# Performance work log

Hardware: AMD Instinct MI355X
Metric: run time of the kernel (lower is better)

The kernel has to match this reference:

```python
import jax, jax.numpy as jnp
import numpy as np
from itertools import combinations as _comb
from jax import lax

RANKS_HIGH = 15
SUITS_HIGH = 5
NA = 6
M = 512
UNSPOOL_INDEX = np.array([h + b for h in _comb(range(0, 4), 2) for b in _comb(range(4, 9), 3)])  # (60,5)


def _unspool(x):
    # x: (B, M, 18) int -> sorted (B, M, 60, 5) rank/suit sequences
    ranks = x[:, :, 0::2]
    suits = x[:, :, 1::2]
    hr, hs = ranks[:, :, :4], suits[:, :, :4]
    br, bs = ranks[:, :, 4:], suits[:, :, 4:]
    hi = jnp.argsort(hs, axis=-1)
    bi = jnp.argsort(bs, axis=-1)
    hr = jnp.take_along_axis(hr, hi, axis=-1)
    hs = jnp.take_along_axis(hs, hi, axis=-1)
    br = jnp.take_along_axis(br, bi, axis=-1)
    bs = jnp.take_along_axis(bs, bi, axis=-1)
    hi2 = jnp.argsort(hr, axis=-1)
    bi2 = jnp.argsort(br, axis=-1)
    ranks_s = jnp.concatenate([jnp.take_along_axis(hr, hi2, -1), jnp.take_along_axis(br, bi2, -1)], axis=-1)
    suits_s = jnp.concatenate([jnp.take_along_axis(hs, hi2, -1), jnp.take_along_axis(bs, bi2, -1)], axis=-1)
    return ranks_s[:, :, UNSPOOL_INDEX], suits_s[:, :, UNSPOOL_INDEX]


def _bn_relu(x, g, b, eps=1e-5):
    # x: (B, M, 60, C, L); torch applies BN per (i,j) slice with batch=60,
    # so stats are over axes (60, L) independently for each (b, m).
    mu = jnp.mean(x, axis=(2, 4), keepdims=True)
    var = jnp.var(x, axis=(2, 4), keepdims=True)
    y = (x - mu) * lax.rsqrt(var + eps) * g[None, None, None, :, None] + b[None, None, None, :, None]
    return jax.nn.relu(y)


def setup_inputs() -> dict:
    key = jax.random.key(0)
    ks = jax.random.split(key, 24)
    s = 0.05
    inp = {
        "x": jax.random.randint(ks[0], (M, 18), 0, 5, dtype=jnp.int64 if jax.config.jax_enable_x64 else jnp.int32),
        "w_suit": jax.random.normal(ks[1], (16, 5), jnp.float32) * s,
        "b_suit": jnp.zeros((16,), jnp.float32),
        "g_suit": jnp.ones((16,), jnp.float32),
        "be_suit": jnp.zeros((16,), jnp.float32),
        "w_rank": jax.random.normal(ks[2], (16, 5, 5), jnp.float32) * s,
        "b_rank": jnp.zeros((16,), jnp.float32),
        "g_rank": jnp.ones((16,), jnp.float32),
        "be_rank": jnp.zeros((16,), jnp.float32),
        "w_h1": jax.random.normal(ks[3], (16, 32), jnp.float32) * s,
        "b_h1": jnp.zeros((32,), jnp.float32),
        "w_h2": jax.random.normal(ks[4], (32, 32), jnp.float32) * s,
        "b_h2": jnp.zeros((32,), jnp.float32),
        "w_cat": jax.random.normal(ks[5], (512, 7463), jnp.float32) * s,
        "b_cat": jnp.zeros((7463,), jnp.float32),
        "w_o1": jax.random.normal(ks[6], (15360, 512), jnp.float32) * 0.01,
        "b_o1": jnp.zeros((512,), jnp.float32),
        "w_o2": jax.random.normal(ks[7], (512, 256), jnp.float32) * s,
        "b_o2": jnp.zeros((256,), jnp.float32),
        "w_o3": jax.random.normal(ks[8], (256, 127), jnp.float32) * s,
        "b_o3": jnp.zeros((127,), jnp.float32),
        "w_sc": jax.random.normal(ks[9], (128, NA), jnp.float32) * s,
        "b_sc": jnp.zeros((NA,), jnp.float32),
    }
    return inp


def reference(x, w_suit, b_suit, g_suit, be_suit, w_rank, b_rank, g_rank, be_rank,
              w_h1, b_h1, w_h2, b_h2, w_cat, b_cat,
              w_o1, b_o1, w_o2, b_o2, w_o3, b_o3, w_sc, b_sc):
    x = x[None]  # (1, M, 18)
    B, Mdim, _ = x.shape
    ranks, suits = _unspool(x)  # (B,M,60,5) each
    hot_ranks = jax.nn.one_hot(ranks, RANKS_HIGH, dtype=jnp.float32)  # (B,M,60,5,15)
    hot_suits = jax.nn.one_hot(suits, SUITS_HIGH, dtype=jnp.float32)  # (B,M,60,5,5)

    # suit conv: Conv1d(5,16,k=1) == channel mixing pointwise
    s_out = jnp.einsum('bmncl,oc->bmnol', hot_suits, w_suit) + b_suit[None, None, None, :, None]
    s_out = _bn_relu(s_out, g_suit, be_suit)  # (B,M,60,16,5)

    # rank conv: Conv1d(5,16,k=5), valid padding: 15 -> 11
    xr = hot_ranks.reshape(B * Mdim * 60, 5, RANKS_HIGH)
    r = lax.conv_general_dilated(xr, w_rank, window_strides=(1,), padding='VALID',
                                 dimension_numbers=('NCH', 'OIH', 'NCH'))
    r = r.reshape(B, Mdim, 60, 16, 11) + b_rank[None, None, None, :, None]
    r_out = _bn_relu(r, g_rank, be_rank)  # (B,M,60,16,11)

    out = jnp.concatenate([r_out, s_out], axis=-1)  # (B,M,60,16,16)
    raw_flat = out.reshape(B, Mdim, 60, 256)

    h = jax.nn.relu(jnp.einsum('...i,io->...o', out, w_h1) + b_h1)
    h = jax.nn.relu(jnp.einsum('...i,io->...o', h, w_h2) + b_h2)  # (B,M,60,16,32)
    logits = jnp.einsum('bmnd,dk->bmnk', h.reshape(B, Mdim, 60, 512), w_cat) + b_cat  # (B,M,60,7463)
    classes = jnp.argmax(logits, axis=-1)  # (B,M,60)
    best_hand = jnp.min(classes, axis=-1)[..., None].astype(jnp.float32)  # (B,M,1)

    rr = raw_flat.reshape(B, Mdim, 60 * 256)  # (B,M,15360)
    rr = jax.nn.relu(rr @ w_o1 + b_o1)
    rr = jax.nn.relu(rr @ w_o2 + b_o2)
    rr = jax.nn.relu(rr @ w_o3 + b_o3)  # (B,M,127)

    final = jnp.concatenate([rr, best_hand], axis=-1).reshape(Mdim, 128)
    return final @ w_sc + b_sc  # (M, nA)
```

## Files before the change

### kernel.cpp

```cpp
#include <hip/hip_runtime.h>


typedef __attribute__((ext_vector_type(8))) short short8;
typedef __attribute__((ext_vector_type(8))) unsigned short ushort8;
typedef __attribute__((ext_vector_type(4))) float f32x4;

#define NCLS  7463
#define NPAD  7680
#define NTILE 30
#define RAWK  15360
#define TAU   2.0e-4f

#define OFF_RAW   0ull
#define OFF_A     31457280ull
#define OFF_B     94371840ull
#define OFF_T2    110100480ull
#define OFF_RR1   124846080ull
#define OFF_CLS   125894656ull
#define OFF_LIST  126017536ull
#define OFF_CNT   126140416ull

__device__ __constant__ signed char HC2[6][2] = {{0,1},{0,2},{0,3},{1,2},{1,3},{2,3}};
__device__ __constant__ signed char BC3[10][3] = {{4,5,6},{4,5,7},{4,5,8},{4,6,7},{4,6,8},
                                                  {4,7,8},{5,6,7},{5,6,8},{5,7,8},{6,7,8}};

__device__ __forceinline__ unsigned short f2bf(float x) {
    unsigned int u = __float_as_uint(x);
    unsigned int r = (u + 0x7fffu + ((u >> 16) & 1u)) >> 16;
    return (unsigned short)r;
}
__device__ __forceinline__ float bf2f(unsigned short b) {
    return __uint_as_float(((unsigned int)b) << 16);
}

__device__ __forceinline__ void gl2lds16(const void* g, void* l) {
    __builtin_amdgcn_global_load_lds(
        (const __attribute__((address_space(1))) unsigned int*)g,
        (__attribute__((address_space(3))) unsigned int*)l, 16, 0, 0);
}

__global__ __launch_bounds__(256) void k0_pack(const float* __restrict__ w_cat,
                                               char* __restrict__ bpack)
{
    const int t = threadIdx.x;
    const int col = blockIdx.x * 64 + (t & 63);
    const int kb  = blockIdx.y * 64 + (t >> 6) * 16;
    float vals[16];
#pragma unroll
    for (int i = 0; i < 16; ++i)
        vals[i] = (col < NCLS) ? w_cat[(size_t)(kb + i) * NCLS + col] : 0.f;
    char* rp = bpack + (size_t)col * 2048 + (size_t)(kb >> 3) * 32;
#pragma unroll
    for (int c = 0; c < 2; ++c) {
        ushort8 hi8, lo8;
#pragma unroll
        for (int j = 0; j < 8; ++j) {
            float x = vals[c * 8 + j];
            unsigned short hb = f2bf(x);
            float hf = bf2f(hb);
            unsigned short lb = f2bf(x - hf);
            hi8[j] = hb; lo8[j] = lb;
        }
        *(ushort8*)(rp + c * 32)      = hi8;
        *(ushort8*)(rp + c * 32 + 16) = lo8;
    }
}

__global__ __launch_bounds__(256) void k1_features(
    const int* __restrict__ x,
    const float* __restrict__ w_suit, const float* __restrict__ b_suit,
    const float* __restrict__ g_suit, const float* __restrict__ be_suit,
    const float* __restrict__ w_rank, const float* __restrict__ b_rank,
    const float* __restrict__ g_rank, const float* __restrict__ be_rank,
    const float* __restrict__ w_h1, const float* __restrict__ b_h1,
    const float* __restrict__ w_h2, const float* __restrict__ b_h2,
    float* __restrict__ raw, char* __restrict__ apack)
{
    __shared__ float s_wrank[400], s_wsuit[80];
    __shared__ float s_brank[16], s_bsuit[16];
    __shared__ float s_wh1[512], s_bh1[32], s_wh2[1024], s_bh2[32];
    __shared__ int   s_sr[9], s_ss[9];
    __shared__ float s_pr_sum[256], s_pr_sq[256], s_ps_sum[256], s_ps_sq[256];
    __shared__ float s_scale_r[16], s_shift_r[16], s_scale_s[16], s_shift_s[16];

    const int t = threadIdx.x;
    const int m = blockIdx.x;
    const int o = t & 15;

    for (int i = t; i < 400;  i += 256) s_wrank[i] = w_rank[i];
    for (int i = t; i < 80;   i += 256) s_wsuit[i] = w_suit[i];
    for (int i = t; i < 512;  i += 256) s_wh1[i]   = w_h1[i];
    for (int i = t; i < 1024; i += 256) s_wh2[i]   = w_h2[i];
    if (t < 16) { s_brank[t] = b_rank[t]; s_bsuit[t] = b_suit[t]; }
    if (t < 32) { s_bh1[t] = b_h1[t]; s_bh2[t] = b_h2[t]; }

    if (t == 0) {
        int r[9], s[9];
        for (int c = 0; c < 9; ++c) { r[c] = x[m*18 + 2*c]; s[c] = x[m*18 + 2*c + 1]; }
        for (int i = 1; i < 4; ++i) {
            int kr = r[i], ks = s[i], key = kr*16 + ks, j = i - 1;
            while (j >= 0 && (r[j]*16 + s[j]) > key) { r[j+1]=r[j]; s[j+1]=s[j]; --j; }
            r[j+1]=kr; s[j+1]=ks;
        }
        for (int i = 5; i < 9; ++i) {
            int kr = r[i], ks = s[i], key = kr*16 + ks, j = i - 1;
            while (j >= 4 && (r[j]*16 + s[j]) > key) { r[j+1]=r[j]; s[j+1]=s[j]; --j; }
            r[j+1]=kr; s[j+1]=ks;
        }
        for (int c = 0; c < 9; ++c) { s_sr[c] = r[c]; s_ss[c] = s[c]; }
    }
    __syncthreads();

    float rv[4][11], sv[4][5];
    float pr_sum = 0.f, pr_sq = 0.f, ps_sum = 0.f, ps_sq = 0.f;
#pragma unroll
    for (int u = 0; u < 4; ++u) {
        const int p = t + u*256;
        if (p < 960) {
            const int n = p >> 4;
            const int hi = n / 10, bi = n % 10;
            int cr[5], cs[5];
            cr[0] = s_sr[HC2[hi][0]]; cs[0] = s_ss[HC2[hi][0]];
            cr[1] = s_sr[HC2[hi][1]]; cs[1] = s_ss[HC2[hi][1]];
            cr[2] = s_sr[BC3[bi][0]]; cs[2] = s_ss[BC3[bi][0]];
            cr[3] = s_sr[BC3[bi][1]]; cs[3] = s_ss[BC3[bi][1]];
            cr[4] = s_sr[BC3[bi][2]]; cs[4] = s_ss[BC3[bi][2]];
            const float br = s_brank[o];
#pragma unroll
            for (int j = 0; j < 11; ++j) {
                float v = br;
#pragma unroll
                for (int c = 0; c < 5; ++c) {
                    const int k = cr[c] - j;
                    if (k >= 0 && k < 5) v += s_wrank[(o*5 + c)*5 + k];
                }
                rv[u][j] = v; pr_sum += v; pr_sq += v*v;
            }
            const float bs = s_bsuit[o];
#pragma unroll
            for (int l = 0; l < 5; ++l) {
                float v = bs;
#pragma unroll
                for (int c = 0; c < 5; ++c) if (cs[c] == l) v += s_wsuit[o*5 + c];
                sv[u][l] = v; ps_sum += v; ps_sq += v*v;
            }
        } else {
#pragma unroll
            for (int j = 0; j < 11; ++j) rv[u][j] = 0.f;
#pragma unroll
            for (int l = 0; l < 5; ++l)  sv[u][l] = 0.f;
        }
    }
    s_pr_sum[t] = pr_sum; s_pr_sq[t] = pr_sq; s_ps_sum[t] = ps_sum; s_ps_sq[t] = ps_sq;
    __syncthreads();

    if (t < 16) {
        float sr = 0.f, sqr = 0.f, ss2 = 0.f, sqs = 0.f;
        for (int slot = 0; slot < 16; ++slot) {
            sr  += s_pr_sum[slot*16 + t];
            sqr += s_pr_sq [slot*16 + t];
            ss2 += s_ps_sum[slot*16 + t];
            sqs += s_ps_sq [slot*16 + t];
        }
        const float nr = 1.f / 660.f, ns = 1.f / 300.f;
        const float mr = sr * nr,  varr = sqr * nr - mr*mr;
        const float ms = ss2 * ns, vars = sqs * ns - ms*ms;
        const float scr = g_rank[t] * rsqrtf(varr + 1e-5f);
        const float scs = g_suit[t] * rsqrtf(vars + 1e-5f);
        s_scale_r[t] = scr; s_shift_r[t] = be_rank[t] - mr * scr;
        s_scale_s[t] = scs; s_shift_s[t] = be_suit[t] - ms * scs;
    }
    __syncthreads();

    const float sc_r = s_scale_r[o], sh_r = s_shift_r[o];
    const float sc_s = s_scale_s[o], sh_s = s_shift_s[o];
#pragma unroll
    for (int u = 0; u < 4; ++u) {
        const int p = t + u*256;
        if (p < 960) {
            const int n = p >> 4;
            float v[16];
#pragma unroll
            for (int j = 0; j < 11; ++j) v[j]    = fmaxf(rv[u][j]*sc_r + sh_r, 0.f);
#pragma unroll
            for (int l = 0; l < 5; ++l)  v[11+l] = fmaxf(sv[u][l]*sc_s + sh_s, 0.f);
            float* rawp = raw + ((size_t)m*15360 + n*256 + o*16);
#pragma unroll
            for (int j = 0; j < 16; ++j) rawp[j] = v[j];
            float hh[32];
#pragma unroll
            for (int jj = 0; jj < 32; ++jj) {
                float a = s_bh1[jj];
#pragma unroll
                for (int i = 0; i < 16; ++i) a = fmaf(v[i], s_wh1[i*32 + jj], a);
                hh[jj] = fmaxf(a, 0.f);
            }
            char* rowp = apack + (size_t)(m*60 + n) * 2048 + o * 128;
#pragma unroll
            for (int c4 = 0; c4 < 4; ++c4) {
                ushort8 hi8, lo8;
#pragma unroll
                for (int j = 0; j < 8; ++j) {
                    const int jj = c4*8 + j;
                    float a = s_bh2[jj];
#pragma unroll
                    for (int i = 0; i < 32; ++i) a = fmaf(hh[i], s_wh2[i*32 + jj], a);
                    float xv = fmaxf(a, 0.f);
                    unsigned short hb = f2bf(xv);
                    float hf = bf2f(hb);
                    unsigned short lb = f2bf(xv - hf);
                    hi8[j] = hb; lo8[j] = lb;
                }
                *(ushort8*)(rowp + c4*32)      = hi8;
                *(ushort8*)(rowp + c4*32 + 16) = lo8;
            }
        }
    }
}

#define STAGE_K2(BB, K) do {                                                  \
    _Pragma("unroll")                                                         \
    for (int i_ = 0; i_ < 4; ++i_) {                                          \
        gl2lds16(aS[i_] + (K)*128, &s_lds[(BB) + dA[i_]]);                    \
        gl2lds16(bS[i_] + (K)*128, &s_lds[(BB) + 32768 + dA[i_]]);            \
    }                                                                         \
} while (0)

#define COMPUTE_K2(BB) do {                                                   \
    short8 ah[8], al[8];                                                      \
    _Pragma("unroll")                                                         \
    for (int fr = 0; fr < 8; ++fr) {                                          \
        const int row_ = wr*128 + fr*16 + (lane & 15);                        \
        const int ba_ = (BB) + row_*128 + (((lane >> 4) * 32) ^ ((row_ & 7) << 4)); \
        ah[fr] = *(const short8*)&s_lds[ba_];                                 \
        al[fr] = *(const short8*)&s_lds[ba_ ^ 16];                            \
    }                                                                         \
    __builtin_amdgcn_s_setprio(1);                                            \
    _Pragma("unroll")                                                         \
    for (int fc = 0; fc < 4; ++fc) {                                          \
        const int col_ = wc*64 + fc*16 + (lane & 15);                         \
        const int bb_ = (BB) + 32768 + col_*128 + (((lane >> 4) * 32) ^ ((col_ & 7) << 4)); \
        const short8 bh = *(const short8*)&s_lds[bb_];                        \
        const short8 bl = *(const short8*)&s_lds[bb_ ^ 16];                   \
        _Pragma("unroll")                                                     \
        for (int fr = 0; fr < 8; ++fr)                                        \
            acc[fr][fc] = __builtin_amdgcn_mfma_f32_16x16x32_bf16(ah[fr], bh, acc[fr][fc], 0, 0, 0); \
        _Pragma("unroll")                                                     \
        for (int fr = 0; fr < 8; ++fr)                                        \
            acc[fr][fc] = __builtin_amdgcn_mfma_f32_16x16x32_bf16(al[fr], bh, acc[fr][fc], 0, 0, 0); \
        _Pragma("unroll")                                                     \
        for (int fr = 0; fr < 8; ++fr)                                        \
            acc[fr][fc] = __builtin_amdgcn_mfma_f32_16x16x32_bf16(ah[fr], bl, acc[fr][fc], 0, 0, 0); \
    }                                                                         \
    __builtin_amdgcn_s_setprio(0);                                            \
} while (0)

__global__ __launch_bounds__(512, 2) void k2_mfma(
    const char* __restrict__ apack, const char* __restrict__ bpack,
    const float* __restrict__ b_cat, uint4* __restrict__ top2buf)
{
    __shared__ __align__(16) unsigned char s_lds[131072];
    const int t = threadIdx.x;
    const int lane = t & 63;
    const int w  = t >> 6;
    const int wr = w >> 2, wc = w & 3;

    const int bid = blockIdx.x;
    const int swz = (bid & 7) * 450 + (bid >> 3);
    const int brow = swz % 120, bcol = swz / 120;
    const int row0 = brow * 256;
    const int col0 = bcol * 256;

    const char* aS[4]; const char* bS[4]; int dA[4];
#pragma unroll
    for (int i = 0; i < 4; ++i) {
        const int c = i*512 + t, r = c >> 3, s = c & 7;
        aS[i] = apack + (size_t)(row0 + r) * 2048 + ((s ^ (r & 7)) << 4);
        bS[i] = bpack + (size_t)(col0 + r) * 2048 + ((s ^ (r & 7)) << 4);
        dA[i] = (i*512 + (t & 448)) * 16;
    }

    f32x4 acc[8][4] = {};

    STAGE_K2(0, 0);
    asm volatile("s_waitcnt vmcnt(0)" ::: "memory");
    __builtin_amdgcn_s_barrier();
    __builtin_amdgcn_sched_barrier(0);

    int cur = 0;
#pragma unroll 1
    for (int it = 0; it < 16; ++it) {
        if (it < 15) STAGE_K2(cur ^ 65536, it + 1);
        COMPUTE_K2(cur);
        asm volatile("s_waitcnt vmcnt(0)" ::: "memory");
        __builtin_amdgcn_s_barrier();
        __builtin_amdgcn_sched_barrier(0);
        cur ^= 65536;
    }

    uint4* sm = (uint4*)s_lds;
#pragma unroll
    for (int fr = 0; fr < 8; ++fr) {
#pragma unroll
        for (int reg = 0; reg < 4; ++reg) {
            float v1 = -3.0e38f, v2 = -3.0e38f;
            int   i1 = 0x7fffffff, i2 = 0x7fffffff;
#pragma unroll
            for (int fc = 0; fc < 4; ++fc) {
                const int colg = col0 + wc*64 + fc*16 + (lane & 15);
                const float v = (colg < NCLS) ? (acc[fr][fc][reg] + b_cat[colg]) : -3.0e38f;
                if (v > v1 || (v == v1 && colg < i1)) { v2=v1; i2=i1; v1=v; i1=colg; }
                else if (v > v2 || (v == v2 && colg < i2)) { v2=v; i2=colg; }
            }
#pragma unroll
            for (int off = 1; off < 16; off <<= 1) {
                const float w1 = __shfl_xor(v1, off, 64); const int j1 = __shfl_xor(i1, off, 64);
                const float w2 = __shfl_xor(v2, off, 64); const int j2 = __shfl_xor(i2, off, 64);
                if (w1 > v1 || (w1 == v1 && j1 < i1)) { v2=v1; i2=i1; v1=w1; i1=j1; }
                else if (w1 > v2 || (w1 == v2 && j1 < i2)) { v2=w1; i2=j1; }
                if (w2 > v1 || (w2 == v1 && j2 < i1)) { v2=v1; i2=i1; v1=w2; i1=j2; }
                else if (w2 > v2 || (w2 == v2 && j2 < i2)) { v2=w2; i2=j2; }
            }
            if ((lane & 15) == 0) {
                const int rl = wr*128 + fr*16 + (lane >> 4)*4 + reg;
                sm[rl*4 + wc] = make_uint4(__float_as_uint(v1), (unsigned)i1,
                                           __float_as_uint(v2), (unsigned)i2);
            }
        }
    }
    __syncthreads();
    if (t < 256) {
        float v1 = -3.0e38f, v2 = -3.0e38f;
        int   i1 = 0x7fffffff, i2 = 0x7fffffff;
#pragma unroll
        for (int q = 0; q < 4; ++q) {
            const uint4 e = sm[t*4 + q];
            const float a1 = __uint_as_float(e.x); const int b1 = (int)e.y;
            const float a2 = __uint_as_float(e.z); const int b2 = (int)e.w;
            if (a1 > v1 || (a1 == v1 && b1 < i1)) { v2=v1; i2=i1; v1=a1; i1=b1; }
            else if (a1 > v2 || (a1 == v2 && b1 < i2)) { v2=a1; i2=b1; }
            if (a2 > v1 || (a2 == v1 && b2 < i1)) { v2=v1; i2=i1; v1=a2; i1=b2; }
            else if (a2 > v2 || (a2 == v2 && b2 < i2)) { v2=a2; i2=b2; }
        }
        top2buf[(size_t)(row0 + t) * NTILE + bcol] =
            make_uint4(__float_as_uint(v1), (unsigned)i1, __float_as_uint(v2), (unsigned)i2);
    }
}

__global__ __launch_bounds__(256) void k2b_reduce(
    const uint4* __restrict__ top2buf, unsigned int* __restrict__ cls,
    unsigned int* __restrict__ list, unsigned int* __restrict__ cnt)
{
    const int row = blockIdx.x * 256 + threadIdx.x;
    float v1 = -3.0e38f, v2 = -3.0e38f;
    int   i1 = 0x7fffffff, i2 = 0x7fffffff;
    for (int tc = 0; tc < NTILE; ++tc) {
        const uint4 e = top2buf[(size_t)row * NTILE + tc];
        const float a1 = __uint_as_float(e.x); const int b1 = (int)e.y;
        const float a2 = __uint_as_float(e.z); const int b2 = (int)e.w;
        if (a1 > v1 || (a1 == v1 && b1 < i1)) { v2=v1; i2=i1; v1=a1; i1=b1; }
        else if (a1 > v2 || (a1 == v2 && b1 < i2)) { v2=a1; i2=b1; }
        if (a2 > v1 || (a2 == v1 && b2 < i1)) { v2=v1; i2=i1; v1=a2; i1=b2; }
        else if (a2 > v2 || (a2 == v2 && b2 < i2)) { v2=a2; i2=b2; }
    }
    cls[row] = (unsigned)i1;
    if (v1 - v2 <= TAU) {
        const unsigned s = atomicAdd(cnt, 1u);
        list[s] = (unsigned)row;
    }
}

__global__ __launch_bounds__(256) void k2c_fixup(
    const char* __restrict__ apack, const char* __restrict__ bpack,
    const float* __restrict__ b_cat, const uint4* __restrict__ top2buf,
    const unsigned int* __restrict__ list, const unsigned int* __restrict__ cnt,
    unsigned int* __restrict__ cls)
{
    __shared__ float h[512];
    __shared__ float s_bv[4];
    __shared__ int   s_bi[4];
    const int t = threadIdx.x, lane = t & 63, wid = t >> 6;
    const int n = (int)*cnt;
    for (int idx = blockIdx.x; idx < n; idx += 1024) {
        const int row = (int)list[idx];
        __syncthreads();
        if (t < 64) {
            const ushort8 hi = *(const ushort8*)(apack + (size_t)row*2048 + t*32);
            const ushort8 lo = *(const ushort8*)(apack + (size_t)row*2048 + t*32 + 16);
#pragma unroll
            for (int j = 0; j < 8; ++j) h[t*8 + j] = bf2f(hi[j]) + bf2f(lo[j]);
        }
        __syncthreads();
        float bv = -3.0e38f; int bi = 0x7fffffff;
        for (int c = wid; c < 60; c += 4) {
            const uint4 e = top2buf[(size_t)row * NTILE + (c >> 1)];
            const int colc = (c & 1) ? (int)e.w : (int)e.y;
            const ushort8 bh = *(const ushort8*)(bpack + (size_t)colc*2048 + lane*32);
            const ushort8 bl = *(const ushort8*)(bpack + (size_t)colc*2048 + lane*32 + 16);
            float p = 0.f;
#pragma unroll
            for (int j = 0; j < 8; ++j) p += h[lane*8 + j] * (bf2f(bh[j]) + bf2f(bl[j]));
#pragma unroll
            for (int off = 1; off < 64; off <<= 1) p += __shfl_xor(p, off, 64);
            const float v = p + b_cat[colc];
            if (v > bv || (v == bv && colc < bi)) { bv = v; bi = colc; }
        }
        if (lane == 0) { s_bv[wid] = bv; s_bi[wid] = bi; }
        __syncthreads();
        if (t == 0) {
            float V = s_bv[0]; int I = s_bi[0];
#pragma unroll
            for (int wv = 1; wv < 4; ++wv)
                if (s_bv[wv] > V || (s_bv[wv] == V && s_bi[wv] < I)) { V = s_bv[wv]; I = s_bi[wv]; }
            cls[row] = (unsigned)I;
        }
    }
}

__global__ __launch_bounds__(256) void k3_rr1(
    const float* __restrict__ raw, const float* __restrict__ w_o1,
    float* __restrict__ rr1)
{
    __shared__ __align__(16) float Alds[16*64];
    __shared__ __align__(16) float Blds[16*64];
    const int t = threadIdx.x;
    const int row0 = blockIdx.x * 64;
    const int col0 = blockIdx.y * 64;
    const int ks   = blockIdx.z * 1920;

    float acc[4][4];
#pragma unroll
    for (int i = 0; i < 4; ++i)
#pragma unroll
        for (int j = 0; j < 4; ++j) acc[i][j] = 0.f;

    const int arow = t >> 2, akq = (t & 3) * 4;
    const int bk   = t >> 4, bc  = (t & 15) * 4;
    const float* Ag = raw  + (size_t)(row0 + arow) * RAWK + ks + akq;
    const float* Bg = w_o1 + (size_t)(ks + bk) * 512 + col0 + bc;

    for (int kc = 0; kc < 120; ++kc) {
        __syncthreads();
        const float4 a = *(const float4*)(Ag + kc*16);
        Alds[(akq+0)*64 + arow] = a.x;  Alds[(akq+1)*64 + arow] = a.y;
        Alds[(akq+2)*64 + arow] = a.z;  Alds[(akq+3)*64 + arow] = a.w;
        *(float4*)&Blds[bk*64 + bc] = *(const float4*)(Bg + (size_t)kc*16*512);
        __syncthreads();

        const int r0 = (t >> 4) * 4, c0 = (t & 15) * 4;
#pragma unroll
        for (int k = 0; k < 16; ++k) {
            float4 a4 = *(const float4*)&Alds[k*64 + r0];
            float4 b4 = *(const float4*)&Blds[k*64 + c0];
            acc[0][0]=fmaf(a4.x,b4.x,acc[0][0]); acc[0][1]=fmaf(a4.x,b4.y,acc[0][1]);
            acc[0][2]=fmaf(a4.x,b4.z,acc[0][2]); acc[0][3]=fmaf(a4.x,b4.w,acc[0][3]);
            acc[1][0]=fmaf(a4.y,b4.x,acc[1][0]); acc[1][1]=fmaf(a4.y,b4.y,acc[1][1]);
            acc[1][2]=fmaf(a4.y,b4.z,acc[1][2]); acc[1][3]=fmaf(a4.y,b4.w,acc[1][3]);
            acc[2][0]=fmaf(a4.z,b4.x,acc[2][0]); acc[2][1]=fmaf(a4.z,b4.y,acc[2][1]);
            acc[2][2]=fmaf(a4.z,b4.z,acc[2][2]); acc[2][3]=fmaf(a4.z,b4.w,acc[2][3]);
            acc[3][0]=fmaf(a4.w,b4.x,acc[3][0]); acc[3][1]=fmaf(a4.w,b4.y,acc[3][1]);
            acc[3][2]=fmaf(a4.w,b4.z,acc[3][2]); acc[3][3]=fmaf(a4.w,b4.w,acc[3][3]);
        }
    }
    const int r0 = (t >> 4) * 4, c0 = (t & 15) * 4;
#pragma unroll
    for (int i = 0; i < 4; ++i)
#pragma unroll
        for (int j = 0; j < 4; ++j)
            atomicAdd(&rr1[(size_t)(row0 + r0 + i)*512 + col0 + c0 + j], acc[i][j]);
}

__global__ __launch_bounds__(256) void k4_tail(
    const float* __restrict__ rr1, const float* __restrict__ b_o1,
    const unsigned int* __restrict__ cls,
    const float* __restrict__ w_o2, const float* __restrict__ b_o2,
    const float* __restrict__ w_o3, const float* __restrict__ b_o3,
    const float* __restrict__ w_sc, const float* __restrict__ b_sc,
    float* __restrict__ out)
{
    __shared__ float s1[512];
    __shared__ float s2[256];
    __shared__ float sf[128];
    __shared__ int s_best;
    const int t = threadIdx.x;
    const int m = blockIdx.x;

    if (t == 0) s_best = 0x7FFFFFFF;
    __syncthreads();
    for (int i = t; i < 512; i += 256)
        s1[i] = fmaxf(rr1[(size_t)m*512 + i] + b_o1[i], 0.f);
    if (t < 60) atomicMin(&s_best, (int)cls[m*60 + t]);
    __syncthreads();
    {
        float a = b_o2[t];
        for (int i = 0; i < 512; ++i) a = fmaf(s1[i], w_o2[i*256 + t], a);
        s2[t] = fmaxf(a, 0.f);
    }
    __syncthreads();
    if (t < 127) {
        float a = b_o3[t];
        for (int i = 0; i < 256; ++i) a = fmaf(s2[i], w_o3[i*127 + t], a);
        sf[t] = fmaxf(a, 0.f);
    }
    if (t == 0) sf[127] = (float)s_best;
    __syncthreads();
    if (t < 6) {
        float a = b_sc[t];
        for (int i = 0; i < 128; ++i) a = fmaf(sf[i], w_sc[i*6 + t], a);
        out[m*6 + t] = a;
    }
}

extern "C" void kernel_launch(void* const* d_in, const int* in_sizes, int n_in,
                              void* d_out, int out_size, void* d_ws, size_t ws_size,
                              hipStream_t stream)
{
    const int*   x       = (const int*)  d_in[0];
    const float* w_suit  = (const float*)d_in[1];
    const float* b_suit  = (const float*)d_in[2];
    const float* g_suit  = (const float*)d_in[3];
    const float* be_suit = (const float*)d_in[4];
    const float* w_rank  = (const float*)d_in[5];
    const float* b_rank  = (const float*)d_in[6];
    const float* g_rank  = (const float*)d_in[7];
    const float* be_rank = (const float*)d_in[8];
    const float* w_h1    = (const float*)d_in[9];
    const float* b_h1    = (const float*)d_in[10];
    const float* w_h2    = (const float*)d_in[11];
    const float* b_h2    = (const float*)d_in[12];
    const float* w_cat   = (const float*)d_in[13];
    const float* b_cat   = (const float*)d_in[14];
    const float* w_o1    = (const float*)d_in[15];
    const float* b_o1    = (const float*)d_in[16];
    const float* w_o2    = (const float*)d_in[17];
    const float* b_o2    = (const float*)d_in[18];
    const float* w_o3    = (const float*)d_in[19];
    const float* b_o3    = (const float*)d_in[20];
    const float* w_sc    = (const float*)d_in[21];
    const float* b_sc    = (const float*)d_in[22];
    float* out = (float*)d_out;

    char* ws = (char*)d_ws;
    float* raw   = (float*)(ws + OFF_RAW);
    char*  apack = ws + OFF_A;
    char*  bpack = ws + OFF_B;
    uint4* top2  = (uint4*)(ws + OFF_T2);
    float* rr1   = (float*)(ws + OFF_RR1);
    unsigned int* cls  = (unsigned int*)(ws + OFF_CLS);
    unsigned int* list = (unsigned int*)(ws + OFF_LIST);
    unsigned int* cnt  = (unsigned int*)(ws + OFF_CNT);

    hipMemsetAsync(rr1, 0, 512*512*sizeof(float), stream);
    hipMemsetAsync(cnt, 0, 256, stream);

    k0_pack<<<dim3(120, 8), 256, 0, stream>>>(w_cat, bpack);
    k1_features<<<512, 256, 0, stream>>>(x, w_suit, b_suit, g_suit, be_suit,
                                         w_rank, b_rank, g_rank, be_rank,
                                         w_h1, b_h1, w_h2, b_h2, raw, apack);
    k2_mfma<<<3600, 512, 0, stream>>>(apack, bpack, b_cat, top2);
    k2b_reduce<<<120, 256, 0, stream>>>(top2, cls, list, cnt);
    k2c_fixup<<<1024, 256, 0, stream>>>(apack, bpack, b_cat, top2, list, cnt, cls);
    k3_rr1<<<dim3(8, 8, 8), 256, 0, stream>>>(raw, w_o1, rr1);
    k4_tail<<<512, 256, 0, stream>>>(rr1, b_o1, cls, w_o2, b_o2, w_o3, b_o3,
                                     w_sc, b_sc, out);
}
```

Baseline: 1.701 ms.

## Interleave staggered LDS prefetch with wave-group compute in MFMA GEMM main loop

```diff
diff --git a/kernel.cpp b/kernel.cpp
--- a/kernel.cpp
+++ b/kernel.cpp
@@ -218,39 +218,43 @@
     }
 }
 
-#define STAGE_K2(BB, K) do {                                                  \
-    _Pragma("unroll")                                                         \
-    for (int i_ = 0; i_ < 4; ++i_) {                                          \
-        gl2lds16(aS[i_] + (K)*128, &s_lds[(BB) + dA[i_]]);                    \
-        gl2lds16(bS[i_] + (K)*128, &s_lds[(BB) + 32768 + dA[i_]]);            \
-    }                                                                         \
+#define K2_SYNC(N) do {                                                       \
+    asm volatile("s_waitcnt vmcnt(" #N ")" ::: "memory");                     \
+    __builtin_amdgcn_s_barrier();                                             \
+    __builtin_amdgcn_sched_barrier(0);                                        \
 } while (0)
 
-#define COMPUTE_K2(BB) do {                                                   \
-    short8 ah[8], al[8];                                                      \
+#define K2_READ_A(CUR) do {                                                   \
     _Pragma("unroll")                                                         \
     for (int fr = 0; fr < 8; ++fr) {                                          \
         const int row_ = wr*128 + fr*16 + (lane & 15);                        \
-        const int ba_ = (BB) + row_*128 + (((lane >> 4) * 32) ^ ((row_ & 7) << 4)); \
+        const int ba_ = (CUR) + row_*128 + (((lane >> 4) * 32) ^ ((row_ & 7) << 4)); \
         ah[fr] = *(const short8*)&s_lds[ba_];                                 \
         al[fr] = *(const short8*)&s_lds[ba_ ^ 16];                            \
+    }                                                                         \
+} while (0)
+
+#define K2_READ_B_MFMA(CUR) do {                                              \
+    short8 bh[4], bl[4];                                                      \
+    _Pragma("unroll")                                                         \
+    for (int fc = 0; fc < 4; ++fc) {                                          \
+        const int col_ = wc*64 + fc*16 + (lane & 15);                         \
+        const int bb_ = (CUR) + 32768 + col_*128 + (((lane >> 4) * 32) ^ ((col_ & 7) << 4)); \
+        bh[fc] = *(const short8*)&s_lds[bb_];                                 \
+        bl[fc] = *(const short8*)&s_lds[bb_ ^ 16];                            \
     }                                                                         \
     __builtin_amdgcn_s_setprio(1);                                            \
     _Pragma("unroll")                                                         \
     for (int fc = 0; fc < 4; ++fc) {                                          \
-        const int col_ = wc*64 + fc*16 + (lane & 15);                         \
-        const int bb_ = (BB) + 32768 + col_*128 + (((lane >> 4) * 32) ^ ((col_ & 7) << 4)); \
-        const short8 bh = *(const short8*)&s_lds[bb_];                        \
-        const short8 bl = *(const short8*)&s_lds[bb_ ^ 16];                   \
         _Pragma("unroll")                                                     \
         for (int fr = 0; fr < 8; ++fr)                                        \
-            acc[fr][fc] = __builtin_amdgcn_mfma_f32_16x16x32_bf16(ah[fr], bh, acc[fr][fc], 0, 0, 0); \
+            acc[fr][fc] = __builtin_amdgcn_mfma_f32_16x16x32_bf16(ah[fr], bh[fc], acc[fr][fc], 0, 0, 0); \
         _Pragma("unroll")                                                     \
         for (int fr = 0; fr < 8; ++fr)                                        \
-            acc[fr][fc] = __builtin_amdgcn_mfma_f32_16x16x32_bf16(al[fr], bh, acc[fr][fc], 0, 0, 0); \
+            acc[fr][fc] = __builtin_amdgcn_mfma_f32_16x16x32_bf16(al[fr], bh[fc], acc[fr][fc], 0, 0, 0); \
         _Pragma("unroll")                                                     \
         for (int fr = 0; fr < 8; ++fr)                                        \
-            acc[fr][fc] = __builtin_amdgcn_mfma_f32_16x16x32_bf16(ah[fr], bl, acc[fr][fc], 0, 0, 0); \
+            acc[fr][fc] = __builtin_amdgcn_mfma_f32_16x16x32_bf16(ah[fr], bl[fc], acc[fr][fc], 0, 0, 0); \
     }                                                                         \
     __builtin_amdgcn_s_setprio(0);                                            \
 } while (0)
@@ -263,7 +267,7 @@
     const int t = threadIdx.x;
     const int lane = t & 63;
     const int w  = t >> 6;
-    const int wr = w >> 2, wc = w & 3;
+    const int wr = w & 1, wc = w >> 1;
 
     const int bid = blockIdx.x;
     const int swz = (bid & 7) * 450 + (bid >> 3);
@@ -282,20 +286,45 @@
 
     f32x4 acc[8][4] = {};
 
-    STAGE_K2(0, 0);
-    asm volatile("s_waitcnt vmcnt(0)" ::: "memory");
-    __builtin_amdgcn_s_barrier();
-    __builtin_amdgcn_sched_barrier(0);
+    gl2lds16(aS[0], &s_lds[dA[0]]);            gl2lds16(aS[1], &s_lds[dA[1]]);
+    gl2lds16(aS[2], &s_lds[dA[2]]);            gl2lds16(aS[3], &s_lds[dA[3]]);
+    gl2lds16(bS[0], &s_lds[32768 + dA[0]]);    gl2lds16(bS[1], &s_lds[32768 + dA[1]]);
+    gl2lds16(bS[2], &s_lds[32768 + dA[2]]);    gl2lds16(bS[3], &s_lds[32768 + dA[3]]);
 
     int cur = 0;
 #pragma unroll 1
-    for (int it = 0; it < 16; ++it) {
-        if (it < 15) STAGE_K2(cur ^ 65536, it + 1);
-        COMPUTE_K2(cur);
-        asm volatile("s_waitcnt vmcnt(0)" ::: "memory");
-        __builtin_amdgcn_s_barrier();
-        __builtin_amdgcn_sched_barrier(0);
-        cur ^= 65536;
+    for (int it = 0; it < 15; ++it) {
+        const int nxt  = cur ^ 65536;
+        const int koff = (it + 1) * 128;
+        short8 ah[8], al[8];
+        K2_SYNC(6);
+        if (wr == 0) K2_READ_A(cur);
+        gl2lds16(aS[0] + koff, &s_lds[nxt + dA[0]]);
+        gl2lds16(aS[1] + koff, &s_lds[nxt + dA[1]]);
+        K2_SYNC(6);
+        if (wr == 1) K2_READ_A(cur);
+        gl2lds16(aS[2] + koff, &s_lds[nxt + dA[2]]);
+        gl2lds16(aS[3] + koff, &s_lds[nxt + dA[3]]);
+        K2_SYNC(6);
+        if (wc < 2) K2_READ_B_MFMA(cur);
+        gl2lds16(bS[0] + koff, &s_lds[nxt + 32768 + dA[0]]);
+        gl2lds16(bS[1] + koff, &s_lds[nxt + 32768 + dA[1]]);
+        K2_SYNC(6);
+        if (wc >= 2) K2_READ_B_MFMA(cur);
+        gl2lds16(bS[2] + koff, &s_lds[nxt + 32768 + dA[2]]);
+        gl2lds16(bS[3] + koff, &s_lds[nxt + 32768 + dA[3]]);
+        cur = nxt;
+    }
+    {
+        short8 ah[8], al[8];
+        K2_SYNC(6);
+        if (wr == 0) K2_READ_A(cur);
+        K2_SYNC(4);
+        if (wr == 1) K2_READ_A(cur);
+        K2_SYNC(2);
+        if (wc < 2) K2_READ_B_MFMA(cur);
+        K2_SYNC(0);
+        if (wc >= 2) K2_READ_B_MFMA(cur);
     }
 
     uint4* sm = (uint4*)s_lds;
```

After: 1.892 ms. 1.11x slower.
